# Performance work log

Hardware: AMD Instinct MI355X
Metric: run time of the kernel (lower is better)

The kernel has to match this reference:

```python
import jax, jax.numpy as jnp
import numpy as np

B, S, FIN, D, H, F = 128, 128, 16, 128, 8, 512
LP, LC = 8, 2          # particle blocks, class blocks
L = LP + LC
DH = D // H
EPS = 1e-5
BN_SCALE = float(1.0 / np.sqrt(1.0 + EPS))  # eval-mode BatchNorm, default init (mean=0, var=1, g=1, b=0)


def _ln(x, g, b):
    m = jnp.mean(x, axis=-1, keepdims=True)
    v = jnp.mean(jnp.square(x - m), axis=-1, keepdims=True)
    return (x - m) * jax.lax.rsqrt(v + EPS) * g + b


def _gelu(x):
    return jax.nn.gelu(x, approximate=False)  # torch nn.GELU default = exact erf


def _interaction_bias(p4, ie_w0, ie_b0, ie_w1, ie_b1, ie_w2, ie_b2):
    # p4: [B,S,4] -> pairwise physics features [B,4,S,S] -> 1x1-conv chain -> [B,H,S,S]
    px, py, pz, e = p4[..., 0], p4[..., 1], p4[..., 2], p4[..., 3]
    pt = jnp.sqrt(px ** 2 + py ** 2)                                  # [B,S]
    rap = 0.5 * jnp.log1p(2.0 * pz / jnp.clip(e - pz, 1e-20, None))   # rapidity
    phi = jnp.arctan2(py, px)
    pi = np.pi
    # index i over axis -2, j over axis -1 (matches xi=unsqueeze(-1), xj=unsqueeze(-2))
    dphi = jnp.mod(phi[:, None, :] - phi[:, :, None] + pi, 2.0 * pi) - pi  # phi_j - phi_i
    drap = rap[:, :, None] - rap[:, None, :]
    delta = jnp.clip(jnp.sqrt(drap ** 2 + dphi ** 2), 1e-8, None)
    ptmin = jnp.minimum(pt[:, :, None], pt[:, None, :])
    kt = jnp.clip(ptmin * delta, 1e-8, None)
    z = jnp.clip(ptmin / jnp.clip(pt[:, :, None] + pt[:, None, :], 1e-8, None), 1e-8, None)
    es = e[:, :, None] + e[:, None, :]
    pxs = px[:, :, None] + px[:, None, :]
    pys = py[:, :, None] + py[:, None, :]
    pzs = pz[:, :, None] + pz[:, None, :]
    m2 = jnp.clip(es ** 2 - pxs ** 2 - pys ** 2 - pzs ** 2, 1e-8, None)
    feat = jnp.log(jnp.stack([delta, kt, z, m2], axis=1))  # [B,4,S,S]
    feat = jax.lax.stop_gradient(feat)  # torch computes this under no_grad
    u = feat.reshape(B, 4, S * S) * BN_SCALE
    u = _gelu((jnp.einsum('oc,bcn->bon', ie_w0, u) + ie_b0[:, None]) * BN_SCALE)
    u = _gelu((jnp.einsum('oc,bcn->bon', ie_w1, u) + ie_b1[:, None]) * BN_SCALE)
    u = _gelu((jnp.einsum('oc,bcn->bon', ie_w2, u) + ie_b2[:, None]) * BN_SCALE)
    return u.reshape(B, H, S, S)


def _mha(q_in, kv_in, wq, wk, wv, wo, gam_h, kpm, bias):
    b, tq = q_in.shape[0], q_in.shape[1]
    q = (q_in @ wq.T).reshape(b, tq, H, DH).transpose(0, 2, 1, 3)
    k = (kv_in @ wk.T).reshape(b, -1, H, DH).transpose(0, 2, 1, 3)
    v = (kv_in @ wv.T).reshape(b, -1, H, DH).transpose(0, 2, 1, 3)
    scores = jnp.einsum('bhqd,bhkd->bhqk', q, k) / np.sqrt(DH)
    if bias is not None:
        scores = scores + bias
    scores = jnp.where(kpm[:, None, None, :], -jnp.inf, scores)
    a = jax.nn.softmax(scores, axis=-1)
    ws = jnp.einsum('bhqk,bhkd->bhqd', a, v) * gam_h[None, :, None, None]  # head-scale gamma
    ws = ws.transpose(0, 2, 1, 3).reshape(b, tq, D)
    return ws @ wo.T


def reference(x, p4, pe_w0, pe_b0, pe_w1, pe_b1, pe_w2, pe_b2,
              ie_w0, ie_b0, ie_w1, ie_b1, ie_w2, ie_b2,
              wq, wk, wv, wo, gam, ln_g, ln_b, lnfc_g, lnfc_b,
              fc1_w, fc1_b, fc2_w, fc2_b, lam, ct, fc_w, fc_b, fin_w, fin_b):
    kpm = x[:, :, 0] == 0.0  # [B,S] key padding mask
    # --- particle feature embedding (BatchNorm eval + [LN, Linear, GELU]x3) ---
    h = x * BN_SCALE
    for w, b in ((pe_w0, pe_b0), (pe_w1, pe_b1), (pe_w2, pe_b2)):
        h = _gelu(_ln(h, 1.0, 0.0) @ w.T + b)
    # --- interaction matrix embedding -> attention bias [B,H,S,S] ---
    bias = _interaction_bias(p4, ie_w0, ie_b0, ie_w1, ie_b1, ie_w2, ie_b2)
    # --- particle attention blocks ---
    xp = h
    for i in range(LP):
        res = xp
        hh = _ln(xp, ln_g[i, 0], ln_b[i, 0])
        a = _mha(hh, hh, wq[i], wk[i], wv[i], wo[i], gam[i], kpm, bias)
        xp = _ln(a, ln_g[i, 1], ln_b[i, 1]) + res
        hh = _ln(xp, ln_g[i, 2], ln_b[i, 2])
        hh = _gelu(hh @ fc1_w[i].T + fc1_b[i])
        hh = _ln(hh, lnfc_g[i], lnfc_b[i])
        xp = (hh @ fc2_w[i].T + fc2_b[i]) + lam[i] * xp
    # --- class attention blocks ---
    xc = jnp.broadcast_to(ct, (B, 1, D))
    kpm2 = jnp.concatenate([jnp.zeros((B, 1), bool), kpm], axis=1)
    for i in range(LP, L):
        res = xc
        xx = _ln(jnp.concatenate([xc, xp], axis=1), ln_g[i, 0], ln_b[i, 0])
        # NOTE: query is the raw (un-normalized) class token, matching the torch code
        a = _mha(xc, xx, wq[i], wk[i], wv[i], wo[i], gam[i], kpm2, None)
        xc = _ln(a, ln_g[i, 1], ln_b[i, 1]) + res
        hh = _ln(xc, ln_g[i, 2], ln_b[i, 2])
        hh = _gelu(hh @ fc1_w[i].T + fc1_b[i])
        hh = _ln(hh, lnfc_g[i], lnfc_b[i])
        xc = (hh @ fc2_w[i].T + fc2_b[i]) + lam[i] * xc
    out = _ln(xc, 1.0, 0.0)[:, 0, :]
    out = jax.nn.relu(out @ fc_w.T + fc_b)
    logits = out @ fin_w.T + fin_b
    return jax.nn.softmax(logits, axis=1)


def setup_inputs() -> dict:
    key = jax.random.key(0)
    ks = iter(jax.random.split(key, 48))
    def nrm(shape, fan_in):
        return jax.random.normal(next(ks), shape, jnp.float32) / np.sqrt(fan_in)
    x = jax.random.normal(next(ks), (B, S, FIN), jnp.float32)
    # physical 4-vectors: E = sqrt(|p|^2 + m^2) so E > |pz| and rapidity is finite
    p3 = jax.random.normal(next(ks), (B, S, 3), jnp.float32) * 2.0
    mass = jax.random.uniform(next(ks), (B, S), jnp.float32, minval=0.05, maxval=1.0)
    e = jnp.sqrt(jnp.sum(p3 ** 2, axis=-1) + mass ** 2)
    p4 = jnp.concatenate([p3, e[..., None]], axis=-1)
    inp = dict(x=x, p4=p4)
    inp.update(
        pe_w0=nrm((128, FIN), FIN), pe_b0=jnp.zeros((128,), jnp.float32),
        pe_w1=nrm((512, 128), 128), pe_b1=jnp.zeros((512,), jnp.float32),
        pe_w2=nrm((D, 512), 512), pe_b2=jnp.zeros((D,), jnp.float32),
        ie_w0=nrm((64, 4), 4), ie_b0=jnp.zeros((64,), jnp.float32),
        ie_w1=nrm((64, 64), 64), ie_b1=jnp.zeros((64,), jnp.float32),
        ie_w2=nrm((H, 64), 64), ie_b2=jnp.zeros((H,), jnp.float32),
        wq=nrm((L, D, D), D), wk=nrm((L, D, D), D), wv=nrm((L, D, D), D), wo=nrm((L, D, D), D),
        gam=jnp.ones((L, H), jnp.float32),
        ln_g=jnp.ones((L, 3, D), jnp.float32), ln_b=jnp.zeros((L, 3, D), jnp.float32),
        lnfc_g=jnp.ones((L, F), jnp.float32), lnfc_b=jnp.zeros((L, F), jnp.float32),
        fc1_w=nrm((L, F, D), D), fc1_b=jnp.zeros((L, F), jnp.float32),
        fc2_w=nrm((L, D, F), F), fc2_b=jnp.zeros((L, D), jnp.float32),
        lam=jnp.ones((L, D), jnp.float32),
        ct=jax.random.normal(next(ks), (1, 1, D), jnp.float32) * 0.02,
        fc_w=nrm((D, D), D), fc_b=jnp.zeros((D,), jnp.float32),
        fin_w=nrm((2, D), D), fin_b=jnp.zeros((2,), jnp.float32),
    )
    return inp
```

## Files before the change

kernel.cpp:

```cpp
#include <hip/hip_runtime.h>
#include <hip/hip_bf16.h>
#include <math.h>

constexpr int B_  = 128;
constexpr int S_  = 128;
constexpr int FIN_= 16;
constexpr int D_  = 128;
constexpr int H_  = 8;
constexpr int F_  = 512;
constexpr float EPSF = 1e-5f;
constexpr float BN_SCALE_F = 0.99999500003749967f;
constexpr float PI_F  = 3.14159265358979323846f;
constexpr float TWO_PI_F = 6.283185307179586477f;
constexpr float INV_TWO_PI_F = 0.15915494309189533577f;

using short8v = __attribute__((ext_vector_type(8))) short;
using float4v = __attribute__((ext_vector_type(4))) float;

__device__ __forceinline__ float gelu_f(float x) {
    return 0.5f * x * (1.0f + erff(x * 0.70710678118654752f));
}

__device__ __forceinline__ float gelu_fast(float x) {
    float z = fabsf(x) * 0.70710678118654752f;
    float t = __builtin_amdgcn_rcpf(1.0f + 0.3275911f * z);
    float poly = t*(0.254829592f + t*(-0.284496736f + t*(1.421413741f + t*(-1.453152027f + t*1.061405429f))));
    float e = 1.0f - poly * __expf(-z*z);
    float s = (x >= 0.f) ? e : -e;
    return 0.5f * x * (1.0f + s);
}

__device__ __forceinline__ short f2b(float f) {
    union { __hip_bfloat16 h; short s; } u;
    u.h = __float2bfloat16(f);
    return u.s;
}

__global__ __launch_bounds__(256) void prep_kernel(
    const float* __restrict__ x, const float* __restrict__ p4,
    float* __restrict__ prep, float* __restrict__ kpm)
{
    int idx = blockIdx.x * 256 + threadIdx.x;
    float px = p4[(size_t)idx*4 + 0];
    float py = p4[(size_t)idx*4 + 1];
    float pz = p4[(size_t)idx*4 + 2];
    float e  = p4[(size_t)idx*4 + 3];
    float pt = sqrtf(px*px + py*py);
    float den = fmaxf(e - pz, 1e-20f);
    float rap = 0.5f * log1pf(2.0f * pz / den);
    float phi = atan2f(py, px);
    prep[(size_t)idx*3 + 0] = pt;
    prep[(size_t)idx*3 + 1] = rap;
    prep[(size_t)idx*3 + 2] = phi;
    kpm[idx] = (x[(size_t)idx * FIN_] == 0.0f) ? 1.0f : 0.0f;
}

__global__ __launch_bounds__(256) void embed1_kernel(
    const float* __restrict__ x, const float* __restrict__ w0,
    const float* __restrict__ b0, float* __restrict__ e1)
{
    __shared__ float xs[2][16];
    __shared__ float ms[2], rss[2];
    int tid = threadIdx.x;
    int t0 = blockIdx.x * 2;
    if (tid < 32) {
        int t = tid >> 4, kk = tid & 15;
        xs[t][kk] = x[(size_t)(t0 + t) * FIN_ + kk] * BN_SCALE_F;
    }
    __syncthreads();
    if (tid < 2) {
        float s = 0.f;
        #pragma unroll
        for (int kk = 0; kk < 16; ++kk) s += xs[tid][kk];
        float m = s * (1.f/16.f);
        float vs = 0.f;
        #pragma unroll
        for (int kk = 0; kk < 16; ++kk) { float d = xs[tid][kk] - m; vs += d*d; }
        ms[tid] = m;
        rss[tid] = rsqrtf(vs * (1.f/16.f) + EPSF);
    }
    __syncthreads();
    int t = tid >> 7, o = tid & 127;
    float m = ms[t], r = rss[t];
    float acc = b0[o];
    #pragma unroll
    for (int kk = 0; kk < 16; ++kk)
        acc += w0[o*16 + kk] * ((xs[t][kk] - m) * r);
    e1[(size_t)(t0 + t)*128 + o] = gelu_f(acc);
}

template<int ACT, bool HASRES>
__global__ __launch_bounds__(256) void linmm_kernel(
    const float* __restrict__ in, const float* __restrict__ w,
    const float* __restrict__ bias, float* __restrict__ out,
    const float* __restrict__ res, const float* __restrict__ lam,
    int N, int K, int Dout)
{
    __shared__ __align__(16) short As[64*64];
    __shared__ __align__(16) short Bs[64*64];
    int tid = threadIdx.x;
    int n0 = blockIdx.x * 64, o0 = blockIdx.y * 64;
    int lane = tid & 63, wv = tid >> 6;
    int srow = tid >> 2, scc = tid & 3;
    const float* ain = in + (size_t)(n0 + srow)*K + scc*16;
    const float* bin = w  + (size_t)(o0 + srow)*K + scc*16;
    float4v acc[4];
    #pragma unroll
    for (int n = 0; n < 4; ++n) acc[n] = (float4v){0.f,0.f,0.f,0.f};
    int c0 = scc * 2;
    int swz = srow & 7;
    int wrb = srow * 64;
    int arow = (wv << 4) + (lane & 15);
    int kgrp = lane >> 4;

    for (int k0 = 0; k0 < K; k0 += 64) {
        float4 a0 = *(const float4*)(ain + k0);
        float4 a1 = *(const float4*)(ain + k0 + 4);
        float4 a2 = *(const float4*)(ain + k0 + 8);
        float4 a3 = *(const float4*)(ain + k0 + 12);
        float4 g0 = *(const float4*)(bin + k0);
        float4 g1 = *(const float4*)(bin + k0 + 4);
        float4 g2 = *(const float4*)(bin + k0 + 8);
        float4 g3 = *(const float4*)(bin + k0 + 12);
        __syncthreads();
        short8v sa0, sa1, sb0, sb1;
        sa0[0]=f2b(a0.x); sa0[1]=f2b(a0.y); sa0[2]=f2b(a0.z); sa0[3]=f2b(a0.w);
        sa0[4]=f2b(a1.x); sa0[5]=f2b(a1.y); sa0[6]=f2b(a1.z); sa0[7]=f2b(a1.w);
        sa1[0]=f2b(a2.x); sa1[1]=f2b(a2.y); sa1[2]=f2b(a2.z); sa1[3]=f2b(a2.w);
        sa1[4]=f2b(a3.x); sa1[5]=f2b(a3.y); sa1[6]=f2b(a3.z); sa1[7]=f2b(a3.w);
        sb0[0]=f2b(g0.x); sb0[1]=f2b(g0.y); sb0[2]=f2b(g0.z); sb0[3]=f2b(g0.w);
        sb0[4]=f2b(g1.x); sb0[5]=f2b(g1.y); sb0[6]=f2b(g1.z); sb0[7]=f2b(g1.w);
        sb1[0]=f2b(g2.x); sb1[1]=f2b(g2.y); sb1[2]=f2b(g2.z); sb1[3]=f2b(g2.w);
        sb1[4]=f2b(g3.x); sb1[5]=f2b(g3.y); sb1[6]=f2b(g3.z); sb1[7]=f2b(g3.w);
        *(short8v*)&As[wrb + (((c0    ) ^ swz) << 3)] = sa0;
        *(short8v*)&As[wrb + (((c0 + 1) ^ swz) << 3)] = sa1;
        *(short8v*)&Bs[wrb + (((c0    ) ^ swz) << 3)] = sb0;
        *(short8v*)&Bs[wrb + (((c0 + 1) ^ swz) << 3)] = sb1;
        __syncthreads();
        #pragma unroll
        for (int ks = 0; ks < 2; ++ks) {
            int ch = (ks << 2) | kgrp;
            short8v av = *(short8v*)&As[arow*64 + ((ch ^ (arow & 7)) << 3)];
            #pragma unroll
            for (int n = 0; n < 4; ++n) {
                int brow = (n << 4) + (lane & 15);
                short8v bv = *(short8v*)&Bs[brow*64 + ((ch ^ (brow & 7)) << 3)];
                acc[n] = __builtin_amdgcn_mfma_f32_16x16x32_bf16(av, bv, acc[n], 0, 0, 0);
            }
        }
    }
    int colb = lane & 15, rgrp = lane >> 4;
    #pragma unroll
    for (int n = 0; n < 4; ++n) {
        int oo = o0 + (n << 4) + colb;
        float bvv = bias ? bias[oo] : 0.f;
        float lm = HASRES ? lam[oo] : 0.f;
        #pragma unroll
        for (int r = 0; r < 4; ++r) {
            int nn = n0 + (wv << 4) + (rgrp << 2) + r;
            float v = acc[n][r] + bvv;
            if (ACT == 1) v = gelu_f(v);
            if (HASRES) v += lm * res[(size_t)nn*Dout + oo];
            out[(size_t)nn*Dout + oo] = v;
        }
    }
}

__global__ __launch_bounds__(256) void qkv3_kernel(
    const float* __restrict__ in,
    const float* __restrict__ wq, const float* __restrict__ wk, const float* __restrict__ wv,
    float* __restrict__ qo, float* __restrict__ ko, float* __restrict__ vo)
{
    const float* w   = (blockIdx.z == 0) ? wq : (blockIdx.z == 1) ? wk : wv;
    float*       out = (blockIdx.z == 0) ? qo : (blockIdx.z == 1) ? ko : vo;
    const int K = 128, Dout = 128;
    __shared__ __align__(16) short As[64*64];
    __shared__ __align__(16) short Bs[64*64];
    int tid = threadIdx.x;
    int n0 = blockIdx.x * 64, o0 = blockIdx.y * 64;
    int lane = tid & 63, wvv = tid >> 6;
    int srow = tid >> 2, scc = tid & 3;
    const float* ain = in + (size_t)(n0 + srow)*K + scc*16;
    const float* bin = w  + (size_t)(o0 + srow)*K + scc*16;
    float4v acc[4];
    #pragma unroll
    for (int n = 0; n < 4; ++n) acc[n] = (float4v){0.f,0.f,0.f,0.f};
    int c0 = scc * 2;
    int swz = srow & 7;
    int wrb = srow * 64;
    int arow = (wvv << 4) + (lane & 15);
    int kgrp = lane >> 4;

    for (int k0 = 0; k0 < K; k0 += 64) {
        float4 a0 = *(const float4*)(ain + k0);
        float4 a1 = *(const float4*)(ain + k0 + 4);
        float4 a2 = *(const float4*)(ain + k0 + 8);
        float4 a3 = *(const float4*)(ain + k0 + 12);
        float4 g0 = *(const float4*)(bin + k0);
        float4 g1 = *(const float4*)(bin + k0 + 4);
        float4 g2 = *(const float4*)(bin + k0 + 8);
        float4 g3 = *(const float4*)(bin + k0 + 12);
        __syncthreads();
        short8v sa0, sa1, sb0, sb1;
        sa0[0]=f2b(a0.x); sa0[1]=f2b(a0.y); sa0[2]=f2b(a0.z); sa0[3]=f2b(a0.w);
        sa0[4]=f2b(a1.x); sa0[5]=f2b(a1.y); sa0[6]=f2b(a1.z); sa0[7]=f2b(a1.w);
        sa1[0]=f2b(a2.x); sa1[1]=f2b(a2.y); sa1[2]=f2b(a2.z); sa1[3]=f2b(a2.w);
        sa1[4]=f2b(a3.x); sa1[5]=f2b(a3.y); sa1[6]=f2b(a3.z); sa1[7]=f2b(a3.w);
        sb0[0]=f2b(g0.x); sb0[1]=f2b(g0.y); sb0[2]=f2b(g0.z); sb0[3]=f2b(g0.w);
        sb0[4]=f2b(g1.x); sb0[5]=f2b(g1.y); sb0[6]=f2b(g1.z); sb0[7]=f2b(g1.w);
        sb1[0]=f2b(g2.x); sb1[1]=f2b(g2.y); sb1[2]=f2b(g2.z); sb1[3]=f2b(g2.w);
        sb1[4]=f2b(g3.x); sb1[5]=f2b(g3.y); sb1[6]=f2b(g3.z); sb1[7]=f2b(g3.w);
        *(short8v*)&As[wrb + (((c0    ) ^ swz) << 3)] = sa0;
        *(short8v*)&As[wrb + (((c0 + 1) ^ swz) << 3)] = sa1;
        *(short8v*)&Bs[wrb + (((c0    ) ^ swz) << 3)] = sb0;
        *(short8v*)&Bs[wrb + (((c0 + 1) ^ swz) << 3)] = sb1;
        __syncthreads();
        #pragma unroll
        for (int ks = 0; ks < 2; ++ks) {
            int ch = (ks << 2) | kgrp;
            short8v av = *(short8v*)&As[arow*64 + ((ch ^ (arow & 7)) << 3)];
            #pragma unroll
            for (int n = 0; n < 4; ++n) {
                int brow = (n << 4) + (lane & 15);
                short8v bv = *(short8v*)&Bs[brow*64 + ((ch ^ (brow & 7)) << 3)];
                acc[n] = __builtin_amdgcn_mfma_f32_16x16x32_bf16(av, bv, acc[n], 0, 0, 0);
            }
        }
    }
    int colb = lane & 15, rgrp = lane >> 4;
    #pragma unroll
    for (int n = 0; n < 4; ++n) {
        int oo = o0 + (n << 4) + colb;
        #pragma unroll
        for (int r = 0; r < 4; ++r) {
            int nn = n0 + (wvv << 4) + (rgrp << 2) + r;
            out[(size_t)nn*Dout + oo] = acc[n][r];
        }
    }
}

__global__ __launch_bounds__(256) void wo_ln_kernel(
    const float* __restrict__ in, const float* __restrict__ w,
    const float* __restrict__ g, const float* __restrict__ bb,
    const float* __restrict__ res, float* __restrict__ out)
{
    __shared__ __align__(16) short As[64*128];
    __shared__ __align__(16) short Bs[128*128];
    __shared__ float gs[128], bs[128];
    __shared__ float parts[2][64][2];
    int tid = threadIdx.x;
    int n0 = blockIdx.x * 64;

    if (tid < 128) gs[tid] = g[tid];
    else bs[tid - 128] = bb[tid - 128];

    {
        int srow = tid >> 2, scc = tid & 3;
        const float* ap = in + (size_t)(n0 + srow)*128 + scc*32;
        #pragma unroll
        for (int c = 0; c < 4; ++c) {
            float4 t0 = *(const float4*)(ap + c*8);
            float4 t1 = *(const float4*)(ap + c*8 + 4);
            short8v sv;
            sv[0]=f2b(t0.x); sv[1]=f2b(t0.y); sv[2]=f2b(t0.z); sv[3]=f2b(t0.w);
            sv[4]=f2b(t1.x); sv[5]=f2b(t1.y); sv[6]=f2b(t1.z); sv[7]=f2b(t1.w);
            int cc = scc*4 + c;
            *(short8v*)&As[srow*128 + ((cc ^ (srow & 7)) << 3)] = sv;
        }
    }
    {
        int brow = tid & 127, bh = tid >> 7;
        const float* bp = w + (size_t)brow*128 + bh*64;
        #pragma unroll
        for (int c = 0; c < 8; ++c) {
            float4 t0 = *(const float4*)(bp + c*8);
            float4 t1 = *(const float4*)(bp + c*8 + 4);
            short8v sv;
            sv[0]=f2b(t0.x); sv[1]=f2b(t0.y); sv[2]=f2b(t0.z); sv[3]=f2b(t0.w);
            sv[4]=f2b(t1.x); sv[5]=f2b(t1.y); sv[6]=f2b(t1.z); sv[7]=f2b(t1.w);
            int cc = bh*8 + c;
            *(short8v*)&Bs[brow*128 + ((cc ^ (brow & 7)) << 3)] = sv;
        }
    }
    __syncthreads();

    int lane = tid & 63, w4 = tid >> 6;
    int l15 = lane & 15, kgrp = lane >> 4;
    int rw = w4 >> 1, cw = w4 & 1;
    float4v acc[2][4];
    #pragma unroll
    for (int m = 0; m < 2; ++m)
        #pragma unroll
        for (int n = 0; n < 4; ++n) acc[m][n] = (float4v){0.f,0.f,0.f,0.f};
    #pragma unroll
    for (int ks = 0; ks < 4; ++ks) {
        int ch = ks*4 + kgrp;
        short8v av[2];
        #pragma unroll
        for (int m = 0; m < 2; ++m) {
            int arow = rw*32 + m*16 + l15;
            av[m] = *(short8v*)&As[arow*128 + ((ch ^ (arow & 7)) << 3)];
        }
        #pragma unroll
        for (int n = 0; n < 4; ++n) {
            int brow = cw*64 + n*16 + l15;
            short8v bv = *(short8v*)&Bs[brow*128 + ((ch ^ (brow & 7)) << 3)];
            #pragma unroll
            for (int m = 0; m < 2; ++m)
                acc[m][n] = __builtin_amdgcn_mfma_f32_16x16x32_bf16(av[m], bv, acc[m][n], 0, 0, 0);
        }
    }
    #pragma unroll
    for (int m = 0; m < 2; ++m) {
        #pragma unroll
        for (int r = 0; r < 4; ++r) {
            float s = acc[m][0][r] + acc[m][1][r] + acc[m][2][r] + acc[m][3][r];
            float sq = acc[m][0][r]*acc[m][0][r] + acc[m][1][r]*acc[m][1][r]
                     + acc[m][2][r]*acc[m][2][r] + acc[m][3][r]*acc[m][3][r];
            s  += __shfl_xor(s, 1);  s  += __shfl_xor(s, 2);  s  += __shfl_xor(s, 4);  s  += __shfl_xor(s, 8);
            sq += __shfl_xor(sq, 1); sq += __shfl_xor(sq, 2); sq += __shfl_xor(sq, 4); sq += __shfl_xor(sq, 8);
            if (l15 == 0) {
                int rl = rw*32 + m*16 + kgrp*4 + r;
                parts[cw][rl][0] = s;
                parts[cw][rl][1] = sq;
            }
        }
    }
    __syncthreads();
    #pragma unroll
    for (int m = 0; m < 2; ++m) {
        int rl_base = rw*32 + m*16 + kgrp*4;
        #pragma unroll
        for (int r = 0; r < 4; ++r) {
            int rl = rl_base + r;
            float st = parts[0][rl][0] + parts[1][rl][0];
            float sqt = parts[0][rl][1] + parts[1][rl][1];
            float mean = st * (1.f/128.f);
            float var = sqt * (1.f/128.f) - mean*mean;
            float rs = rsqrtf(fmaxf(var, 0.f) + EPSF);
            size_t rowg = (size_t)(n0 + rl);
            #pragma unroll
            for (int n = 0; n < 4; ++n) {
                int col = cw*64 + n*16 + l15;
                float v = (acc[m][n][r] - mean) * rs * gs[col] + bs[col] + res[rowg*128 + col];
                out[rowg*128 + col] = v;
            }
        }
    }
}

__global__ __launch_bounds__(256) void fc1_ln_kernel(
    const float* __restrict__ in,
    const float* __restrict__ g, const float* __restrict__ bb,
    const float* __restrict__ w1, const float* __restrict__ b1,
    const float* __restrict__ lg, const float* __restrict__ lb,
    float* __restrict__ out)
{
    __shared__ __align__(16) short As[64*128];
    __shared__ __align__(16) short BUF[64*128];
    __shared__ float gs[128], bs[128];
    __shared__ float bs1[512], lgs[512], lbs[512];
    int tid = threadIdx.x;
    int n0 = blockIdx.x * 64;
    int srow = tid >> 2, scc = tid & 3;

    if (tid < 128) gs[tid] = g ? g[tid] : 1.f;
    else bs[tid - 128] = bb ? bb[tid - 128] : 0.f;
    for (int idx = tid; idx < 512; idx += 256) {
        bs1[idx] = b1[idx];
        lgs[idx] = lg ? lg[idx] : 1.f;
        lbs[idx] = lb ? lb[idx] : 0.f;
    }

    {
        const float* ap = in + (size_t)(n0 + srow)*128 + scc*32;
        float vals[32];
        float s = 0.f, sq = 0.f;
        #pragma unroll
        for (int q8 = 0; q8 < 8; ++q8) {
            float4 t4 = *(const float4*)(ap + q8*4);
            vals[q8*4+0]=t4.x; vals[q8*4+1]=t4.y; vals[q8*4+2]=t4.z; vals[q8*4+3]=t4.w;
            s += t4.x + t4.y + t4.z + t4.w;
            sq += t4.x*t4.x + t4.y*t4.y + t4.z*t4.z + t4.w*t4.w;
        }
        s  += __shfl_xor(s, 1);  s  += __shfl_xor(s, 2);
        sq += __shfl_xor(sq, 1); sq += __shfl_xor(sq, 2);
        float mean = s * (1.f/128.f);
        float var = sq * (1.f/128.f) - mean*mean;
        float rs = rsqrtf(fmaxf(var, 0.f) + EPSF);
        __syncthreads();
        #pragma unroll
        for (int c = 0; c < 4; ++c) {
            short8v sv;
            #pragma unroll
            for (int e = 0; e < 8; ++e) {
                int k = scc*32 + c*8 + e;
                sv[e] = f2b((vals[c*8+e] - mean) * rs * gs[k] + bs[k]);
            }
            int cc = scc*4 + c;
            *(short8v*)&As[srow*128 + ((cc ^ (srow & 7)) << 3)] = sv;
        }
    }
    __syncthreads();

    int lane = tid & 63, w4 = tid >> 6;
    int l15 = lane & 15, kgrp = lane >> 4;
    int arow = (w4 << 4) + l15;
    short8v aF[4];
    #pragma unroll
    for (int ks = 0; ks < 4; ++ks) {
        int ch = ks*4 + kgrp;
        aF[ks] = *(short8v*)&As[arow*128 + ((ch ^ (arow & 7)) << 3)];
    }
    float4v acc[32];
    #pragma unroll
    for (int n = 0; n < 32; ++n) acc[n] = (float4v){0.f,0.f,0.f,0.f};

    #pragma unroll
    for (int c8 = 0; c8 < 8; ++c8) {
        __syncthreads();
        {
            const float* bp = w1 + (size_t)(c8*64 + srow)*128 + scc*32;
            #pragma unroll
            for (int c = 0; c < 4; ++c) {
                float4 t0 = *(const float4*)(bp + c*8);
                float4 t1 = *(const float4*)(bp + c*8 + 4);
                short8v sv;
                sv[0]=f2b(t0.x); sv[1]=f2b(t0.y); sv[2]=f2b(t0.z); sv[3]=f2b(t0.w);
                sv[4]=f2b(t1.x); sv[5]=f2b(t1.y); sv[6]=f2b(t1.z); sv[7]=f2b(t1.w);
                int cc = scc*4 + c;
                *(short8v*)&BUF[srow*128 + ((cc ^ (srow & 7)) << 3)] = sv;
            }
        }
        __syncthreads();
        #pragma unroll
        for (int ks = 0; ks < 4; ++ks) {
            int ch = ks*4 + kgrp;
            #pragma unroll
            for (int n = 0; n < 4; ++n) {
                int brow = n*16 + l15;
                short8v bv = *(short8v*)&BUF[brow*128 + ((ch ^ (brow & 7)) << 3)];
                acc[c8*4+n] = __builtin_amdgcn_mfma_f32_16x16x32_bf16(aF[ks], bv, acc[c8*4+n], 0, 0, 0);
            }
        }
    }

    #pragma unroll
    for (int nf = 0; nf < 32; ++nf) {
        int col = nf*16 + l15;
        #pragma unroll
        for (int r = 0; r < 4; ++r)
            acc[nf][r] = gelu_f(acc[nf][r] + bs1[col]);
    }
    float mean[4], rsv[4];
    #pragma unroll
    for (int r = 0; r < 4; ++r) {
        float s = 0.f, sq = 0.f;
        #pragma unroll
        for (int nf = 0; nf < 32; ++nf) { float v = acc[nf][r]; s += v; sq += v*v; }
        s  += __shfl_xor(s, 1);  s  += __shfl_xor(s, 2);  s  += __shfl_xor(s, 4);  s  += __shfl_xor(s, 8);
        sq += __shfl_xor(sq, 1); sq += __shfl_xor(sq, 2); sq += __shfl_xor(sq, 4); sq += __shfl_xor(sq, 8);
        mean[r] = s * (1.f/512.f);
        float var = sq * (1.f/512.f) - mean[r]*mean[r];
        rsv[r] = rsqrtf(fmaxf(var, 0.f) + EPSF);
    }
    #pragma unroll
    for (int r = 0; r < 4; ++r) {
        size_t rowg = (size_t)(n0 + (w4 << 4) + (kgrp << 2) + r);
        #pragma unroll
        for (int nf = 0; nf < 32; ++nf) {
            int col = nf*16 + l15;
            out[rowg*512 + col] = (acc[nf][r] - mean[r]) * rsv[r] * lgs[col] + lbs[col];
        }
    }
}

__global__ __launch_bounds__(256) void bias_kernel(
    const float* __restrict__ p4, const float* __restrict__ prep,
    const float* __restrict__ w0, const float* __restrict__ b0,
    const float* __restrict__ w1, const float* __restrict__ b1,
    const float* __restrict__ w2, const float* __restrict__ b2,
    __hip_bfloat16* __restrict__ bias)
{
    __shared__ float pj[128][8];
    __shared__ float w0s[256], b0s[64], b1s[64], b2s[8];
    __shared__ __align__(16) short U[256*64];
    __shared__ __align__(16) short W1s[64*64];
    __shared__ __align__(16) short W2s[16*64];
    __shared__ short si[256], sj[256];
    int tid = threadIdx.x;
    int b  = blockIdx.x / 33;
    int p  = (blockIdx.x % 33) * 256 + tid;

    w0s[tid] = w0[tid];
    if (tid < 64) { b0s[tid] = b0[tid]; b1s[tid] = b1[tid]; }
    if (tid < 8)  b2s[tid] = b2[tid];
    {
        int o = tid >> 2;
        const float* wp = w1 + o*64 + (tid & 3) * 16;
        #pragma unroll
        for (int h2 = 0; h2 < 2; ++h2) {
            float4 t0 = *(const float4*)(wp + h2*8);
            float4 t1 = *(const float4*)(wp + h2*8 + 4);
            short8v sv;
            sv[0]=f2b(t0.x); sv[1]=f2b(t0.y); sv[2]=f2b(t0.z); sv[3]=f2b(t0.w);
            sv[4]=f2b(t1.x); sv[5]=f2b(t1.y); sv[6]=f2b(t1.z); sv[7]=f2b(t1.w);
            int cc = (tid & 3)*2 + h2;
            *(short8v*)&W1s[o*64 + ((cc ^ (o & 7)) << 3)] = sv;
        }
    }
    if (tid < 128) {
        int o2 = tid >> 3, c = tid & 7;
        short8v sv;
        #pragma unroll
        for (int e = 0; e < 8; ++e)
            sv[e] = (o2 < 8) ? f2b(w2[o2*64 + c*8 + e]) : (short)0;
        *(short8v*)&W2s[o2*64 + ((c ^ (o2 & 7)) << 3)] = sv;
    }
    if (tid < 128) {
        int s = tid;
        const float* pr = prep + ((size_t)b*S_ + s)*3;
        pj[s][0] = pr[0]; pj[s][1] = pr[1]; pj[s][2] = pr[2];
        const float* pp = p4 + ((size_t)b*S_ + s)*4;
        pj[s][3] = pp[0]; pj[s][4] = pp[1]; pj[s][5] = pp[2]; pj[s][6] = pp[3];
    }

    bool valid = p < 8256;
    int i = 0, j = 0;
    if (valid) {
        i = (int)((257.0f - sqrtf((float)(66049 - 8*p))) * 0.5f);
        if (i > 127) i = 127;
        if (i < 0) i = 0;
        while (i > 0 && i*(257 - i)/2 > p) --i;
        while ((i + 1)*(257 - (i + 1))/2 <= p) ++i;
        j = i + (p - i*(257 - i)/2);
    }
    si[tid] = (short)(valid ? i : -1);
    sj[tid] = (short)j;
    __syncthreads();
// ... 106 lines not shown
    const float* __restrict__ in, float* __restrict__ out,
    const float* __restrict__ g, const float* __restrict__ bb,
    const float* __restrict__ res)
{
    constexpr int E = W / 64;
    int row = blockIdx.x;
    int lane = threadIdx.x;
    const float* r = in + (size_t)row * W;
    float vals[E];
    float s = 0.f;
    #pragma unroll
    for (int e = 0; e < E; ++e) { vals[e] = r[lane + 64*e]; s += vals[e]; }
    #pragma unroll
    for (int o = 32; o > 0; o >>= 1) s += __shfl_xor(s, o);
    float m = s * (1.f / W);
    float vsum = 0.f;
    #pragma unroll
    for (int e = 0; e < E; ++e) { float d = vals[e] - m; vsum += d*d; }
    #pragma unroll
    for (int o = 32; o > 0; o >>= 1) vsum += __shfl_xor(vsum, o);
    float rs = rsqrtf(vsum * (1.f / W) + EPSF);
    #pragma unroll
    for (int e = 0; e < E; ++e) {
        int c = lane + 64*e;
        float v = (vals[e] - m) * rs;
        if (g) v = v * g[c] + bb[c];
        if (res) v += res[(size_t)row*W + c];
        out[(size_t)row*W + c] = v;
    }
}

__global__ __launch_bounds__(256) void attn_kernel(
    const float* __restrict__ q, const float* __restrict__ k, const float* __restrict__ v,
    const __hip_bfloat16* __restrict__ bias, const float* __restrict__ kpm,
    const float* __restrict__ gam, int layer, float* __restrict__ out)
{
    int bh = blockIdx.x;
    int b = bh >> 3, h = bh & 7;
    __shared__ __align__(16) short qs[128][40];
    __shared__ __align__(16) short ks[128][40];
    __shared__ __align__(16) short vst[16][136];
    __shared__ __align__(16) short pb[64][136];
    int tid = threadIdx.x;

    {
        int r = tid >> 1, hh = tid & 1;
        const float* qp = q + ((size_t)(b*S_ + r))*D_ + h*16 + hh*8;
        const float* kp = k + ((size_t)(b*S_ + r))*D_ + h*16 + hh*8;
        float4 a0 = *(const float4*)qp;
        float4 a1 = *(const float4*)(qp + 4);
        float4 c0 = *(const float4*)kp;
        float4 c1 = *(const float4*)(kp + 4);
        short8v sq, sk, zz;
        sq[0]=f2b(a0.x); sq[1]=f2b(a0.y); sq[2]=f2b(a0.z); sq[3]=f2b(a0.w);
        sq[4]=f2b(a1.x); sq[5]=f2b(a1.y); sq[6]=f2b(a1.z); sq[7]=f2b(a1.w);
        sk[0]=f2b(c0.x); sk[1]=f2b(c0.y); sk[2]=f2b(c0.z); sk[3]=f2b(c0.w);
        sk[4]=f2b(c1.x); sk[5]=f2b(c1.y); sk[6]=f2b(c1.z); sk[7]=f2b(c1.w);
        #pragma unroll
        for (int e = 0; e < 8; ++e) zz[e] = 0;
        *(short8v*)&qs[r][hh*8] = sq;
        *(short8v*)&ks[r][hh*8] = sk;
        *(short8v*)&qs[r][16 + hh*8] = zz;
        *(short8v*)&ks[r][16 + hh*8] = zz;
    }
    {
        int j = tid >> 1, dg = (tid & 1)*8;
        const float* vp = v + ((size_t)(b*S_ + j))*D_ + h*16 + dg;
        float4 v0 = *(const float4*)vp;
        float4 v1 = *(const float4*)(vp + 4);
        vst[dg+0][j] = f2b(v0.x); vst[dg+1][j] = f2b(v0.y);
        vst[dg+2][j] = f2b(v0.z); vst[dg+3][j] = f2b(v0.w);
        vst[dg+4][j] = f2b(v1.x); vst[dg+5][j] = f2b(v1.y);
        vst[dg+6][j] = f2b(v1.z); vst[dg+7][j] = f2b(v1.w);
    }
    float gm = gam[layer*H_ + h];
    __syncthreads();

    int lane = tid & 63, w = tid >> 6;
    int l15 = lane & 15, l4 = lane >> 4;

    float msk[8];
    #pragma unroll
    for (int n = 0; n < 8; ++n) msk[n] = kpm[b*S_ + n*16 + l15];

    #pragma unroll
    for (int half = 0; half < 2; ++half) {
        int mrow = half*64 + w*16;
        short8v aq = *(short8v*)&qs[mrow + l15][l4*8];
        float4v sf[8];
        #pragma unroll
        for (int n = 0; n < 8; ++n) {
            short8v bk = *(short8v*)&ks[n*16 + l15][l4*8];
            sf[n] = __builtin_amdgcn_mfma_f32_16x16x32_bf16(aq, bk, (float4v){0.f,0.f,0.f,0.f}, 0, 0, 0);
        }
        #pragma unroll
        for (int r = 0; r < 4; ++r) {
            int srow = mrow + l4*4 + r;
            const __hip_bfloat16* bp = bias + ((size_t)(b*H_ + h)*S_ + srow)*S_ + l15;
            float sc[8];
            float mx = -1e30f;
            #pragma unroll
            for (int n = 0; n < 8; ++n) {
                float s = sf[n][r]*0.25f + __bfloat162float(bp[n*16]);
                if (msk[n] != 0.f) s = -1e30f;
                sc[n] = s;
                mx = fmaxf(mx, s);
            }
            mx = fmaxf(mx, __shfl_xor(mx, 1));
            mx = fmaxf(mx, __shfl_xor(mx, 2));
            mx = fmaxf(mx, __shfl_xor(mx, 4));
            mx = fmaxf(mx, __shfl_xor(mx, 8));
            float sum = 0.f;
            #pragma unroll
            for (int n = 0; n < 8; ++n) { float e = __expf(sc[n] - mx); sc[n] = e; sum += e; }
            sum += __shfl_xor(sum, 1);
            sum += __shfl_xor(sum, 2);
            sum += __shfl_xor(sum, 4);
            sum += __shfl_xor(sum, 8);
            float inv = 1.f / sum;
            int lrow = w*16 + l4*4 + r;
            #pragma unroll
            for (int n = 0; n < 8; ++n)
                pb[lrow][n*16 + l15] = f2b(sc[n] * inv);
        }
        float4v of = (float4v){0.f,0.f,0.f,0.f};
        #pragma unroll
        for (int ks4 = 0; ks4 < 4; ++ks4) {
            short8v pa = *(short8v*)&pb[w*16 + l15][ks4*32 + l4*8];
            short8v vb = *(short8v*)&vst[l15][ks4*32 + l4*8];
            of = __builtin_amdgcn_mfma_f32_16x16x32_bf16(pa, vb, of, 0, 0, 0);
        }
        #pragma unroll
        for (int r = 0; r < 4; ++r)
            out[((size_t)(b*S_ + mrow + l4*4 + r))*D_ + h*16 + l15] = of[r] * gm;
    }
}

__global__ __launch_bounds__(256) void cattn_kernel(
    const float* __restrict__ qc, const float* __restrict__ kc, const float* __restrict__ vc,
    const float* __restrict__ kpm, const float* __restrict__ gam,
    int layer, float* __restrict__ outc)
{
    int b = blockIdx.x / H_, h = blockIdx.x % H_;
    __shared__ float sc[132];
    int tid = threadIdx.x;
    const int T = S_ + 1;
    if (tid < T) {
        float acc = 0.f;
        #pragma unroll
        for (int d = 0; d < 16; ++d)
            acc += qc[(size_t)b*D_ + h*16 + d] * kc[((size_t)b*T + tid)*D_ + h*16 + d];
        acc *= 0.25f;
        if (tid > 0 && kpm[b*S_ + tid - 1] != 0.f) acc = -1e30f;
        sc[tid] = acc;
    }
    __syncthreads();
    if (tid == 0) {
        float m = -1e30f;
        for (int jj = 0; jj < T; ++jj) m = fmaxf(m, sc[jj]);
        float sum = 0.f;
        for (int jj = 0; jj < T; ++jj) { float e = __expf(sc[jj] - m); sc[jj] = e; sum += e; }
        float inv = 1.f / sum;
        for (int jj = 0; jj < T; ++jj) sc[jj] *= inv;
    }
    __syncthreads();
    if (tid < 16) {
        float acc = 0.f;
        for (int jj = 0; jj < T; ++jj) acc += sc[jj] * vc[((size_t)b*T + jj)*D_ + h*16 + tid];
        outc[(size_t)b*D_ + h*16 + tid] = acc * gam[layer*H_ + h];
    }
}

__global__ __launch_bounds__(256) void bcast_ct_kernel(const float* __restrict__ ct, float* __restrict__ xc)
{
    int idx = blockIdx.x * 256 + threadIdx.x;
    xc[idx] = ct[idx & (D_ - 1)];
}

__global__ __launch_bounds__(256) void concat_kernel(
    const float* __restrict__ xc, const float* __restrict__ xp, float* __restrict__ xx)
{
    int idx = blockIdx.x * 256 + threadIdx.x;
    int d = idx & (D_ - 1);
    int r = idx >> 7;
    int b = r / (S_ + 1);
    int s = r % (S_ + 1);
    xx[idx] = (s == 0) ? xc[(size_t)b*D_ + d] : xp[((size_t)b*S_ + (s - 1))*D_ + d];
}

__global__ __launch_bounds__(128) void head_kernel(
    const float* __restrict__ u, const float* __restrict__ fc_w, const float* __restrict__ fc_b,
    const float* __restrict__ fin_w, const float* __restrict__ fin_b, float* __restrict__ out)
{
    __shared__ float us[128], r0[128], r1[128];
    int b = blockIdx.x, tid = threadIdx.x;
    us[tid] = u[(size_t)b*D_ + tid];
    __syncthreads();
    float acc = fc_b[tid];
    for (int kk = 0; kk < 128; ++kk) acc += fc_w[tid*128 + kk] * us[kk];
    float rl = fmaxf(acc, 0.f);
    r0[tid] = fin_w[tid] * rl;
    r1[tid] = fin_w[128 + tid] * rl;
    __syncthreads();
    #pragma unroll
    for (int o = 64; o > 0; o >>= 1) {
        if (tid < o) { r0[tid] += r0[tid + o]; r1[tid] += r1[tid + o]; }
        __syncthreads();
    }
    if (tid == 0) {
        float l0 = r0[0] + fin_b[0], l1 = r1[0] + fin_b[1];
        float m = fmaxf(l0, l1);
        float e0 = __expf(l0 - m), e1 = __expf(l1 - m);
        float inv = 1.f / (e0 + e1);
        out[b*2 + 0] = e0 * inv;
        out[b*2 + 1] = e1 * inv;
    }
}

extern "C" void kernel_launch(void* const* d_in, const int* in_sizes, int n_in,
                              void* d_out, int out_size, void* d_ws, size_t ws_size,
                              hipStream_t stream)
{
    (void)in_sizes; (void)n_in; (void)out_size;
    const float* x     = (const float*)d_in[0];
    const float* p4    = (const float*)d_in[1];
    const float* pe_w0 = (const float*)d_in[2];
    const float* pe_b0 = (const float*)d_in[3];
    const float* pe_w1 = (const float*)d_in[4];
    const float* pe_b1 = (const float*)d_in[5];
    const float* pe_w2 = (const float*)d_in[6];
    const float* pe_b2 = (const float*)d_in[7];
    const float* ie_w0 = (const float*)d_in[8];
    const float* ie_b0 = (const float*)d_in[9];
    const float* ie_w1 = (const float*)d_in[10];
    const float* ie_b1 = (const float*)d_in[11];
    const float* ie_w2 = (const float*)d_in[12];
    const float* ie_b2 = (const float*)d_in[13];
    const float* wq    = (const float*)d_in[14];
    const float* wk    = (const float*)d_in[15];
    const float* wv    = (const float*)d_in[16];
    const float* wo    = (const float*)d_in[17];
    const float* gam   = (const float*)d_in[18];
    const float* ln_g  = (const float*)d_in[19];
    const float* ln_b  = (const float*)d_in[20];
    const float* lnfc_g= (const float*)d_in[21];
    const float* lnfc_b= (const float*)d_in[22];
    const float* fc1_w = (const float*)d_in[23];
    const float* fc1_b = (const float*)d_in[24];
    const float* fc2_w = (const float*)d_in[25];
    const float* fc2_b = (const float*)d_in[26];
    const float* lam   = (const float*)d_in[27];
    const float* ct    = (const float*)d_in[28];
    const float* fc_w  = (const float*)d_in[29];
    const float* fc_b  = (const float*)d_in[30];
    const float* fin_w = (const float*)d_in[31];
    const float* fin_b = (const float*)d_in[32];

    float* ws = (float*)d_ws;
    const size_t o_bias = 0;
    const size_t o_prep = o_bias + 8388608;
    const size_t o_kpm  = o_prep + 49152;
    const size_t o_xp   = o_kpm  + 16384;
    const size_t o_b1   = o_xp   + 2097152;
    const size_t o_b2   = o_b1   + 2097152;
    const size_t o_b3   = o_b2   + 8388608;
    const size_t o_xx   = o_b3   + 2097152;
    const size_t o_xc   = o_xx   + 2113536;
    const size_t o_t1   = o_xc   + 16384;
    const size_t o_t2   = o_t1   + 16384;
    const size_t o_ac   = o_t2   + 65536;
    const size_t o_u    = o_ac   + 16384;
    const size_t o_end  = o_u    + 16384;

    size_t used_bytes = o_end * sizeof(float);
    if (used_bytes > ws_size) used_bytes = ws_size;
    hipMemsetAsync(d_ws, 0, used_bytes, stream);

    __hip_bfloat16* biasb = (__hip_bfloat16*)(ws + o_bias);
    float* prep = ws + o_prep;
    float* kpm  = ws + o_kpm;
    float* xp   = ws + o_xp;
    float* b1   = ws + o_b1;
    float* b2   = ws + o_b2;
    float* b3   = ws + o_b3;
    float* xx   = ws + o_xx;
    float* xc   = ws + o_xc;
    float* t2   = ws + o_t2;
    float* ac   = ws + o_ac;
    float* ufin = ws + o_u;

    const int NT = B_ * S_;
    const int NC = B_ * (S_ + 1);

    prep_kernel<<<NT/256, 256, 0, stream>>>(x, p4, prep, kpm);
    embed1_kernel<<<NT/2, 256, 0, stream>>>(x, pe_w0, pe_b0, b1);
    fc1_ln_kernel<<<NT/64, 256, 0, stream>>>(b1, nullptr, nullptr, pe_w1, pe_b1, nullptr, nullptr, b2);
    linmm_kernel<1,false><<<dim3(NT/64, 2), 256, 0, stream>>>(b2, pe_w2, pe_b2, xp, nullptr, nullptr, NT, 512, 128);
    bias_kernel<<<B_*33, 256, 0, stream>>>(p4, prep, ie_w0, ie_b0, ie_w1, ie_b1, ie_w2, ie_b2, biasb);

    float* qb = b2;
    float* kb = b2 + 2097152;
    float* vb = b2 + 4194304;

    for (int i = 0; i < 8; ++i) {
        const float* g0p = ln_g + (size_t)(i*3 + 0)*D_; const float* b0p = ln_b + (size_t)(i*3 + 0)*D_;
        const float* g1p = ln_g + (size_t)(i*3 + 1)*D_; const float* b1p = ln_b + (size_t)(i*3 + 1)*D_;
        const float* g2p = ln_g + (size_t)(i*3 + 2)*D_; const float* b2p = ln_b + (size_t)(i*3 + 2)*D_;

        ln_kernel<128><<<NT, 64, 0, stream>>>(xp, b1, g0p, b0p, nullptr);
        qkv3_kernel<<<dim3(NT/64, 2, 3), 256, 0, stream>>>(
            b1, wq + (size_t)i*D_*D_, wk + (size_t)i*D_*D_, wv + (size_t)i*D_*D_, qb, kb, vb);
        attn_kernel<<<B_*H_, 256, 0, stream>>>(qb, kb, vb, biasb, kpm, gam, i, b1);
        wo_ln_kernel<<<NT/64, 256, 0, stream>>>(b1, wo + (size_t)i*D_*D_, g1p, b1p, xp, xp);
        fc1_ln_kernel<<<NT/64, 256, 0, stream>>>(xp, g2p, b2p,
            fc1_w + (size_t)i*F_*D_, fc1_b + (size_t)i*F_,
            lnfc_g + (size_t)i*F_, lnfc_b + (size_t)i*F_, b2);
        linmm_kernel<0,true><<<dim3(NT/64, 2), 256, 0, stream>>>(b2, fc2_w + (size_t)i*D_*F_, fc2_b + (size_t)i*D_, xp, xp, lam + (size_t)i*D_, NT, F_, D_);
    }

    bcast_ct_kernel<<<B_*D_/256, 256, 0, stream>>>(ct, xc);
    float* kc = b2;
    float* vc = b2 + 2113536;
    for (int i = 8; i < 10; ++i) {
        const float* g0p = ln_g + (size_t)(i*3 + 0)*D_; const float* b0p = ln_b + (size_t)(i*3 + 0)*D_;
        const float* g1p = ln_g + (size_t)(i*3 + 1)*D_; const float* b1p = ln_b + (size_t)(i*3 + 1)*D_;
        const float* g2p = ln_g + (size_t)(i*3 + 2)*D_; const float* b2p = ln_b + (size_t)(i*3 + 2)*D_;

        concat_kernel<<<(B_*(S_+1)*D_)/256, 256, 0, stream>>>(xc, xp, xx);
        ln_kernel<128><<<NC, 64, 0, stream>>>(xx, xx, g0p, b0p, nullptr);
        linmm_kernel<0,false><<<dim3(NC/64, 2), 256, 0, stream>>>(xx, wk + (size_t)i*D_*D_, nullptr, kc, nullptr, nullptr, NC, D_, D_);
        linmm_kernel<0,false><<<dim3(NC/64, 2), 256, 0, stream>>>(xx, wv + (size_t)i*D_*D_, nullptr, vc, nullptr, nullptr, NC, D_, D_);
        linmm_kernel<0,false><<<dim3(B_/64, 2), 256, 0, stream>>>(xc, wq + (size_t)i*D_*D_, nullptr, b3, nullptr, nullptr, B_, D_, D_);
        cattn_kernel<<<B_*H_, 256, 0, stream>>>(b3, kc, vc, kpm, gam, i, ac);
        wo_ln_kernel<<<B_/64, 256, 0, stream>>>(ac, wo + (size_t)i*D_*D_, g1p, b1p, xc, xc);
        fc1_ln_kernel<<<B_/64, 256, 0, stream>>>(xc, g2p, b2p,
            fc1_w + (size_t)i*F_*D_, fc1_b + (size_t)i*F_,
            lnfc_g + (size_t)i*F_, lnfc_b + (size_t)i*F_, t2);
        linmm_kernel<0,true><<<dim3(B_/64, 2), 256, 0, stream>>>(t2, fc2_w + (size_t)i*D_*F_, fc2_b + (size_t)i*D_, xc, xc, lam + (size_t)i*D_, B_, F_, D_);
    }

    ln_kernel<128><<<B_, 64, 0, stream>>>(xc, ufin, nullptr, nullptr, nullptr);
    head_kernel<<<B_, 128, 0, stream>>>(ufin, fc_w, fc_b, fin_w, fin_b, (float*)d_out);
}
```

Baseline: 1.279 ms.

## Fuse next-layer LayerNorm into FC2 epilogue and merge QKV projections per tile

The FC2 GEMM now computes all 128 output columns per block, so its epilogue can apply bias and the lambda-scaled residual and then run the next block's pre-attention LayerNorm with shuffle reductions. This removes a separate LN kernel launch and one activation read/write per layer. The QKV kernel now keeps the bf16 A tile in registers and loops over the three weight matrices inside one block instead of launching a 3-D grid. This cuts redundant activation loads but gives fewer, larger blocks with more register pressure.

```diff
diff --git a/kernel.cpp b/kernel.cpp
--- a/kernel.cpp
+++ b/kernel.cpp
@@ -166,75 +166,191 @@
     }
 }
 
-__global__ __launch_bounds__(256) void qkv3_kernel(
+__global__ __launch_bounds__(256) void qkvall_kernel(
     const float* __restrict__ in,
     const float* __restrict__ wq, const float* __restrict__ wk, const float* __restrict__ wv,
     float* __restrict__ qo, float* __restrict__ ko, float* __restrict__ vo)
 {
-    const float* w   = (blockIdx.z == 0) ? wq : (blockIdx.z == 1) ? wk : wv;
-    float*       out = (blockIdx.z == 0) ? qo : (blockIdx.z == 1) ? ko : vo;
-    const int K = 128, Dout = 128;
+    __shared__ __align__(16) short As[64*128];
+    __shared__ __align__(16) short Bs[128*64];
+    int tid = threadIdx.x;
+    int n0 = blockIdx.x * 64;
+    int srow = tid >> 2, scc = tid & 3;
+    int lane = tid & 63, w4 = tid >> 6;
+    int l15 = lane & 15, kgrp = lane >> 4;
+
+    {
+        const float* ap = in + (size_t)(n0 + srow)*128 + scc*32;
+        #pragma unroll
+        for (int c = 0; c < 4; ++c) {
+            float4 t0 = *(const float4*)(ap + c*8);
+            float4 t1 = *(const float4*)(ap + c*8 + 4);
+            short8v sv;
+            sv[0]=f2b(t0.x); sv[1]=f2b(t0.y); sv[2]=f2b(t0.z); sv[3]=f2b(t0.w);
+            sv[4]=f2b(t1.x); sv[5]=f2b(t1.y); sv[6]=f2b(t1.z); sv[7]=f2b(t1.w);
+            int cc = scc*4 + c;
+            *(short8v*)&As[srow*128 + ((cc ^ (srow & 7)) << 3)] = sv;
+        }
+    }
+    __syncthreads();
+    int arow = (w4 << 4) + l15;
+    short8v aF[4];
+    #pragma unroll
+    for (int ks = 0; ks < 4; ++ks) {
+        int ch = ks*4 + kgrp;
+        aF[ks] = *(short8v*)&As[arow*128 + ((ch ^ (arow & 7)) << 3)];
+    }
+
+    int brow2 = tid >> 1, half = tid & 1;
+    #pragma unroll
+    for (int wsel = 0; wsel < 3; ++wsel) {
+        const float* w   = (wsel == 0) ? wq : (wsel == 1) ? wk : wv;
+        float*       out = (wsel == 0) ? qo : (wsel == 1) ? ko : vo;
+        float4v acc[8];
+        #pragma unroll
+        for (int n = 0; n < 8; ++n) acc[n] = (float4v){0.f,0.f,0.f,0.f};
+        #pragma unroll
+        for (int c2 = 0; c2 < 2; ++c2) {
+            const float* bp = w + (size_t)brow2*128 + c2*64 + half*32;
+            float4 t[8];
+            #pragma unroll
+            for (int c = 0; c < 8; ++c) t[c] = *(const float4*)(bp + c*4);
+            __syncthreads();
+            #pragma unroll
+            for (int c = 0; c < 4; ++c) {
+                short8v sv;
+                sv[0]=f2b(t[c*2].x);   sv[1]=f2b(t[c*2].y);   sv[2]=f2b(t[c*2].z);   sv[3]=f2b(t[c*2].w);
+                sv[4]=f2b(t[c*2+1].x); sv[5]=f2b(t[c*2+1].y); sv[6]=f2b(t[c*2+1].z); sv[7]=f2b(t[c*2+1].w);
+                int cc = half*4 + c;
+                *(short8v*)&Bs[brow2*64 + ((cc ^ (brow2 & 7)) << 3)] = sv;
+            }
+            __syncthreads();
+            #pragma unroll
+            for (int ksl = 0; ksl < 2; ++ksl) {
+                int chb = ksl*4 + kgrp;
+                short8v av = aF[c2*2 + ksl];
+                #pragma unroll
+                for (int n = 0; n < 8; ++n) {
+                    int brow = n*16 + l15;
+                    short8v bv = *(short8v*)&Bs[brow*64 + ((chb ^ (brow & 7)) << 3)];
+                    acc[n] = __builtin_amdgcn_mfma_f32_16x16x32_bf16(av, bv, acc[n], 0, 0, 0);
+                }
+            }
+        }
+        #pragma unroll
+        for (int n = 0; n < 8; ++n) {
+            int col = n*16 + l15;
+            #pragma unroll
+            for (int r = 0; r < 4; ++r) {
+                int row = n0 + (w4 << 4) + (kgrp << 2) + r;
+                out[(size_t)row*128 + col] = acc[n][r];
+            }
+        }
+    }
+}
+
+template<bool EMITLN>
+__global__ __launch_bounds__(256) void fc2_ln_kernel(
+    const float* __restrict__ in, const float* __restrict__ w,
+    const float* __restrict__ bias2, const float* __restrict__ lam,
+    const float* __restrict__ res, float* __restrict__ out_xp,
+    const float* __restrict__ lng, const float* __restrict__ lnb,
+    float* __restrict__ out_ln)
+{
     __shared__ __align__(16) short As[64*64];
-    __shared__ __align__(16) short Bs[64*64];
+    __shared__ __align__(16) short Bs[128*64];
+    __shared__ float biass[128], lams[128], gs[128], bs[128];
     int tid = threadIdx.x;
-    int n0 = blockIdx.x * 64, o0 = blockIdx.y * 64;
-    int lane = tid & 63, wvv = tid >> 6;
+    int n0 = blockIdx.x * 64;
     int srow = tid >> 2, scc = tid & 3;
-    const float* ain = in + (size_t)(n0 + srow)*K + scc*16;
-    const float* bin = w  + (size_t)(o0 + srow)*K + scc*16;
-    float4v acc[4];
-    #pragma unroll
-    for (int n = 0; n < 4; ++n) acc[n] = (float4v){0.f,0.f,0.f,0.f};
-    int c0 = scc * 2;
-    int swz = srow & 7;
-    int wrb = srow * 64;
-    int arow = (wvv << 4) + (lane & 15);
-    int kgrp = lane >> 4;
-
-    for (int k0 = 0; k0 < K; k0 += 64) {
-        float4 a0 = *(const float4*)(ain + k0);
-        float4 a1 = *(const float4*)(ain + k0 + 4);
-        float4 a2 = *(const float4*)(ain + k0 + 8);
-        float4 a3 = *(const float4*)(ain + k0 + 12);
-        float4 g0 = *(const float4*)(bin + k0);
-        float4 g1 = *(const float4*)(bin + k0 + 4);
-        float4 g2 = *(const float4*)(bin + k0 + 8);
-        float4 g3 = *(const float4*)(bin + k0 + 12);
+    int brow2 = tid >> 1, half = tid & 1;
+    int lane = tid & 63, w4 = tid >> 6;
+    int l15 = lane & 15, kgrp = lane >> 4;
+
+    if (tid < 128) {
+        biass[tid] = bias2[tid];
+        lams[tid]  = lam[tid];
+        if (EMITLN) { gs[tid] = lng[tid]; bs[tid] = lnb[tid]; }
+    }
+
+    float4v acc[8];
+    #pragma unroll
+    for (int n = 0; n < 8; ++n) acc[n] = (float4v){0.f,0.f,0.f,0.f};
+
+    for (int c8 = 0; c8 < 8; ++c8) {
+        const float* ap = in + (size_t)(n0 + srow)*512 + c8*64 + scc*16;
+        float4 a0 = *(const float4*)(ap);
+        float4 a1 = *(const float4*)(ap + 4);
+        float4 a2 = *(const float4*)(ap + 8);
+        float4 a3 = *(const float4*)(ap + 12);
+        const float* bp = w + (size_t)brow2*512 + c8*64 + half*32;
+        float4 t[8];
+        #pragma unroll
+        for (int c = 0; c < 8; ++c) t[c] = *(const float4*)(bp + c*4);
         __syncthreads();
-        short8v sa0, sa1, sb0, sb1;
-        sa0[0]=f2b(a0.x); sa0[1]=f2b(a0.y); sa0[2]=f2b(a0.z); sa0[3]=f2b(a0.w);
-        sa0[4]=f2b(a1.x); sa0[5]=f2b(a1.y); sa0[6]=f2b(a1.z); sa0[7]=f2b(a1.w);
-        sa1[0]=f2b(a2.x); sa1[1]=f2b(a2.y); sa1[2]=f2b(a2.z); sa1[3]=f2b(a2.w);
-        sa1[4]=f2b(a3.x); sa1[5]=f2b(a3.y); sa1[6]=f2b(a3.z); sa1[7]=f2b(a3.w);
-        sb0[0]=f2b(g0.x); sb0[1]=f2b(g0.y); sb0[2]=f2b(g0.z); sb0[3]=f2b(g0.w);
-        sb0[4]=f2b(g1.x); sb0[5]=f2b(g1.y); sb0[6]=f2b(g1.z); sb0[7]=f2b(g1.w);
-        sb1[0]=f2b(g2.x); sb1[1]=f2b(g2.y); sb1[2]=f2b(g2.z); sb1[3]=f2b(g2.w);
-        sb1[4]=f2b(g3.x); sb1[5]=f2b(g3.y); sb1[6]=f2b(g3.z); sb1[7]=f2b(g3.w);
-        *(short8v*)&As[wrb + (((c0    ) ^ swz) << 3)] = sa0;
-        *(short8v*)&As[wrb + (((c0 + 1) ^ swz) << 3)] = sa1;
-        *(short8v*)&Bs[wrb + (((c0    ) ^ swz) << 3)] = sb0;
-        *(short8v*)&Bs[wrb + (((c0 + 1) ^ swz) << 3)] = sb1;
+        {
+            short8v sa0, sa1;
+            sa0[0]=f2b(a0.x); sa0[1]=f2b(a0.y); sa0[2]=f2b(a0.z); sa0[3]=f2b(a0.w);
+            sa0[4]=f2b(a1.x); sa0[5]=f2b(a1.y); sa0[6]=f2b(a1.z); sa0[7]=f2b(a1.w);
+            sa1[0]=f2b(a2.x); sa1[1]=f2b(a2.y); sa1[2]=f2b(a2.z); sa1[3]=f2b(a2.w);
+            sa1[4]=f2b(a3.x); sa1[5]=f2b(a3.y); sa1[6]=f2b(a3.z); sa1[7]=f2b(a3.w);
+            int c0 = scc*2;
+            *(short8v*)&As[srow*64 + (((c0    ) ^ (srow & 7)) << 3)] = sa0;
+            *(short8v*)&As[srow*64 + (((c0 + 1) ^ (srow & 7)) << 3)] = sa1;
+            #pragma unroll
+            for (int c = 0; c < 4; ++c) {
+                short8v sv;
+                sv[0]=f2b(t[c*2].x);   sv[1]=f2b(t[c*2].y);   sv[2]=f2b(t[c*2].z);   sv[3]=f2b(t[c*2].w);
+                sv[4]=f2b(t[c*2+1].x); sv[5]=f2b(t[c*2+1].y); sv[6]=f2b(t[c*2+1].z); sv[7]=f2b(t[c*2+1].w);
+                int cc = half*4 + c;
+                *(short8v*)&Bs[brow2*64 + ((cc ^ (brow2 & 7)) << 3)] = sv;
+            }
+        }
         __syncthreads();
+        int arow = (w4 << 4) + l15;
         #pragma unroll
         for (int ks = 0; ks < 2; ++ks) {
-            int ch = (ks << 2) | kgrp;
+            int ch = ks*4 + kgrp;
             short8v av = *(short8v*)&As[arow*64 + ((ch ^ (arow & 7)) << 3)];
             #pragma unroll
-            for (int n = 0; n < 4; ++n) {
-                int brow = (n << 4) + (lane & 15);
+            for (int n = 0; n < 8; ++n) {
+                int brow = n*16 + l15;
                 short8v bv = *(short8v*)&Bs[brow*64 + ((ch ^ (brow & 7)) << 3)];
                 acc[n] = __builtin_amdgcn_mfma_f32_16x16x32_bf16(av, bv, acc[n], 0, 0, 0);
             }
         }
     }
-    int colb = lane & 15, rgrp = lane >> 4;
-    #pragma unroll
-    for (int n = 0; n < 4; ++n) {
-        int oo = o0 + (n << 4) + colb;
+
+    float v[8][4];
+    #pragma unroll
+    for (int n = 0; n < 8; ++n) {
+        int col = n*16 + l15;
+        float bvv = biass[col], lm = lams[col];
         #pragma unroll
         for (int r = 0; r < 4; ++r) {
-            int nn = n0 + (wvv << 4) + (rgrp << 2) + r;
-            out[(size_t)nn*Dout + oo] = acc[n][r];
+            size_t row = (size_t)(n0 + (w4 << 4) + (kgrp << 2) + r);
+            float vv = acc[n][r] + bvv + lm * res[row*128 + col];
+            v[n][r] = vv;
+            out_xp[row*128 + col] = vv;
+        }
+    }
+    if (EMITLN) {
+        #pragma unroll
+        for (int r = 0; r < 4; ++r) {
+            float s = 0.f, sq = 0.f;
+            #pragma unroll
+            for (int n = 0; n < 8; ++n) { float vv = v[n][r]; s += vv; sq += vv*vv; }
+            s  += __shfl_xor(s, 1);  s  += __shfl_xor(s, 2);  s  += __shfl_xor(s, 4);  s  += __shfl_xor(s, 8);
+            sq += __shfl_xor(sq, 1); sq += __shfl_xor(sq, 2); sq += __shfl_xor(sq, 4); sq += __shfl_xor(sq, 8);
+            float mean = s * (1.f/128.f);
+            float var = sq * (1.f/128.f) - mean*mean;
+            float rs = rsqrtf(fmaxf(var, 0.f) + EPSF);
+            size_t row = (size_t)(n0 + (w4 << 4) + (kgrp << 2) + r);
+            #pragma unroll
+            for (int n = 0; n < 8; ++n) {
+                int col = n*16 + l15;
+                out_ln[row*128 + col] = (v[n][r] - mean) * rs * gs[col] + bs[col];
+            }
         }
     }
 }
@@ -947,20 +1063,30 @@
     float* kb = b2 + 2097152;
     float* vb = b2 + 4194304;
 
+    ln_kernel<128><<<NT, 64, 0, stream>>>(xp, b1, ln_g, ln_b, nullptr);
+
     for (int i = 0; i < 8; ++i) {
-        const float* g0p = ln_g + (size_t)(i*3 + 0)*D_; const float* b0p = ln_b + (size_t)(i*3 + 0)*D_;
         const float* g1p = ln_g + (size_t)(i*3 + 1)*D_; const float* b1p = ln_b + (size_t)(i*3 + 1)*D_;
         const float* g2p = ln_g + (size_t)(i*3 + 2)*D_; const float* b2p = ln_b + (size_t)(i*3 + 2)*D_;
 
-        ln_kernel<128><<<NT, 64, 0, stream>>>(xp, b1, g0p, b0p, nullptr);
-        qkv3_kernel<<<dim3(NT/64, 2, 3), 256, 0, stream>>>(
+        qkvall_kernel<<<NT/64, 256, 0, stream>>>(
             b1, wq + (size_t)i*D_*D_, wk + (size_t)i*D_*D_, wv + (size_t)i*D_*D_, qb, kb, vb);
         attn_kernel<<<B_*H_, 256, 0, stream>>>(qb, kb, vb, biasb, kpm, gam, i, b1);
         wo_ln_kernel<<<NT/64, 256, 0, stream>>>(b1, wo + (size_t)i*D_*D_, g1p, b1p, xp, xp);
         fc1_ln_kernel<<<NT/64, 256, 0, stream>>>(xp, g2p, b2p,
             fc1_w + (size_t)i*F_*D_, fc1_b + (size_t)i*F_,
             lnfc_g + (size_t)i*F_, lnfc_b + (size_t)i*F_, b2);
-        linmm_kernel<0,true><<<dim3(NT/64, 2), 256, 0, stream>>>(b2, fc2_w + (size_t)i*D_*F_, fc2_b + (size_t)i*D_, xp, xp, lam + (size_t)i*D_, NT, F_, D_);
+        if (i < 7) {
+            const float* gn = ln_g + (size_t)((i+1)*3 + 0)*D_;
+            const float* bn = ln_b + (size_t)((i+1)*3 + 0)*D_;
+            fc2_ln_kernel<true><<<NT/64, 256, 0, stream>>>(
+                b2, fc2_w + (size_t)i*D_*F_, fc2_b + (size_t)i*D_, lam + (size_t)i*D_,
+                xp, xp, gn, bn, b1);
+        } else {
+            fc2_ln_kernel<false><<<NT/64, 256, 0, stream>>>(
+                b2, fc2_w + (size_t)i*D_*F_, fc2_b + (size_t)i*D_, lam + (size_t)i*D_,
+                xp, xp, nullptr, nullptr, nullptr);
+        }
     }
 
     bcast_ct_kernel<<<B_*D_/256, 256, 0, stream>>>(ct, xc);
```

New measurement: 1.329 ms. 3.9% more time.
